# Performance work log

Hardware: AMD Instinct MI355X
Metric: run time of the kernel (lower is better)

Reference implementation:

```python
import jax, jax.numpy as jnp
import numpy as np

NUM_HEADS = 16
KERNEL_SIZE = 13


def setup_inputs() -> dict:
    key = jax.random.key(0)
    ks = jax.random.split(key, 6)
    B, L, C = 4, 4096, 512
    H, K = NUM_HEADS, KERNEL_SIZE
    x = jax.random.normal(ks[0], (B, L, C), dtype=jnp.float32)
    qkv_w = jax.random.normal(ks[1], (C, 3 * C), dtype=jnp.float32) * 0.02
    qkv_b = jnp.zeros((3 * C,), dtype=jnp.float32)
    rpb = jax.random.normal(ks[2], (H, 2 * K - 1), dtype=jnp.float32) * 0.02
    proj_w = jax.random.normal(ks[3], (C, C), dtype=jnp.float32) * 0.02
    proj_b = jnp.zeros((C,), dtype=jnp.float32)
    return {"x": x, "qkv_w": qkv_w, "qkv_b": qkv_b, "rpb": rpb,
            "proj_w": proj_w, "proj_b": proj_b}


def reference(x, qkv_w, qkv_b, rpb, proj_w, proj_b):
    B, L, C = x.shape
    H, K = NUM_HEADS, KERNEL_SIZE
    hd = C // H
    scale = hd ** -0.5
    kh = K // 2

    # qkv projection -> q,k,v each [B,H,L,hd]
    qkv = (x @ qkv_w + qkv_b).reshape(B, L, 3, H, hd).transpose(2, 0, 3, 1, 4)
    q, k, v = qkv[0] * scale, qkv[1], qkv[2]

    # NATTEN window: start index clamped so window stays in-bounds
    pos = jnp.arange(L)
    ni = jnp.clip(pos - kh, 0, L - K)              # [L] window start per query
    idx = ni[:, None] + jnp.arange(K)[None, :]     # [L,K] key positions
    # rpb index: (key_pos - query_pos) + (K-1)
    rpb_idx = (ni - pos + (K - 1))[:, None] + jnp.arange(K)[None, :]  # [L,K]

    k_win = k[:, :, idx, :]                        # [B,H,L,K,hd]
    v_win = v[:, :, idx, :]                        # [B,H,L,K,hd]

    attn = jnp.einsum('bhld,bhlkd->bhlk', q, k_win) + rpb[:, rpb_idx][None]
    attn = jax.nn.softmax(attn, axis=-1)

    out = jnp.einsum('bhlk,bhlkd->bhld', attn, v_win)  # [B,H,L,hd]
    out = out.transpose(0, 2, 1, 3).reshape(B, L, C)
    return out @ proj_w + proj_b
```

## Files before the change

### kernel.cpp

```cpp
#include <hip/hip_runtime.h>
#include <hip/hip_bf16.h>
#include <stdint.h>


typedef __attribute__((ext_vector_type(8))) short short8;
typedef __attribute__((ext_vector_type(4))) float f32x4;
typedef __attribute__((ext_vector_type(8))) unsigned short u16x8;
typedef __attribute__((ext_vector_type(4))) float float4v;

#define NB 4
#define NL 4096
#define NC 512
#define NH 16
#define HD 32
#define KW 13
#define KHALF 6
#define NM (NB*NL)

__device__ __forceinline__ float b2f(unsigned short u) {
  union { unsigned int i; float f; } x; x.i = ((unsigned int)u) << 16; return x.f;
}
__device__ __forceinline__ unsigned short f2b(float f) {
  __hip_bfloat16 h = __float2bfloat16(f);
  return __builtin_bit_cast(unsigned short, h);
}
__device__ __forceinline__ void gll16(const void* g, unsigned short* l) {
  __builtin_amdgcn_global_load_lds(
      (const __attribute__((address_space(1))) void*)g,
      (__attribute__((address_space(3))) void*)l, 16, 0, 0);
}
__device__ __forceinline__ short8 pack8(float4v lo, float4v hi) {
  u16x8 u;
  u[0] = f2b(lo.x); u[1] = f2b(lo.y); u[2] = f2b(lo.z); u[3] = f2b(lo.w);
  u[4] = f2b(hi.x); u[5] = f2b(hi.y); u[6] = f2b(hi.z); u[7] = f2b(hi.w);
  return __builtin_bit_cast(short8, u);
}

__global__ __launch_bounds__(256)
void pack_bf(const float* __restrict__ W, unsigned short* __restrict__ Bf,
             int N, int ngroups) {
  int g = blockIdx.x * 256 + threadIdx.x;
  if (g >= ngroups) return;
  int lane = g & 63;
  int kb   = (g >> 6) & 1;
  int nj   = (g >> 7) & 3;
  int wn   = (g >> 9) & 1;
  int kt   = (g >> 10) & 7;
  int tn   = g >> 13;
  int n  = tn * 128 + wn * 64 + nj * 16 + (lane & 15);
  int k0 = kt * 64 + (kb * 4 + (lane >> 4)) * 8;
  u16x8 u;
  #pragma unroll
  for (int e = 0; e < 8; ++e) u[e] = f2b(W[(long)(k0 + e) * N + n]);
  ((u16x8*)Bf)[g] = u;
}

#define BAR() __builtin_amdgcn_s_barrier()
#define LGK0() do { asm volatile("s_waitcnt lgkmcnt(0)" ::: "memory"); \
                    __builtin_amdgcn_sched_barrier(0); } while (0)
#define VM(N) asm volatile("s_waitcnt vmcnt(" #N ")" ::: "memory")

#define LDBG(KT) do { \
  const short8* _bp = (const short8*)(Bfw + (long)(KT) * 8192) + lane; \
  _Pragma("unroll") for (int nj = 0; nj < 4; ++nj) \
    _Pragma("unroll") for (int kb = 0; kb < 2; ++kb) \
      bf[nj][kb] = _bp[(nj*2 + kb) * 64]; \
} while (0)

#define MMA_ALL() do { \
  __builtin_amdgcn_s_setprio(1); \
  _Pragma("unroll") for (int ii = 0; ii < 4; ++ii) \
    _Pragma("unroll") for (int jj = 0; jj < 4; ++jj) \
      _Pragma("unroll") for (int kb = 0; kb < 2; ++kb) \
        acc[ii][jj] = __builtin_amdgcn_mfma_f32_16x16x32_bf16( \
            af[ii][kb], bf[jj][kb], acc[ii][jj], 0, 0, 0); \
  __builtin_amdgcn_s_setprio(0); \
} while (0)


__device__ __forceinline__ void stageA_f32(const float* __restrict__ G,
                                           long rowBase, int K, int kt,
                                           unsigned short* ldsDst, int tid) {
  int lane = tid & 63, w = tid >> 6;
  int rsub = lane >> 4;
  int slot = lane & 15;
  #pragma unroll
  for (int q = 0; q < 8; ++q) {
    int row = w * 32 + q * 4 + rsub;
    int g = slot ^ (row & 15);
    const float* src = G + (rowBase + row) * (long)K + kt * 64 + g * 4;
    gll16(src, ldsDst + row * 128 + slot * 8);
  }
}

#define LDA_F32(ABASE) do { \
  const char* _ba = (const char*)(ABASE); \
  _Pragma("unroll") for (int ii = 0; ii < 4; ++ii) { \
    int _row = wm*64 + ii*16 + lr; \
    const char* _rp = _ba + _row*256; \
    _Pragma("unroll") for (int kb = 0; kb < 2; ++kb) { \
      int _g = (kb*4 + lk) * 2; \
      float4v _lo = *(const float4v*)(_rp + ((_g ^ lr) * 16)); \
      float4v _hi = *(const float4v*)(_rp + (((_g+1) ^ lr) * 16)); \
      af[ii][kb] = pack8(_lo, _hi); \
    } \
  } \
} while (0)

#define G1TILE(ABUF, KT, STG, VMARG) do { \
  LDBG(KT); \
  LDA_F32(ABUF); \
  LGK0(); \
  BAR(); \
  if (STG) stageA_f32(Ag, mBase, K, (KT) + 2, ABUF, tid); \
  VMARG; \
  MMA_ALL(); \
  BAR(); \
} while (0)

__global__ __launch_bounds__(256, 2)
void gemm128f(const float* __restrict__ Ag,
              const unsigned short* __restrict__ Bf,
              const float* __restrict__ bias,
              unsigned short* __restrict__ Cout,
              int M, int N, int K, int tilesN) {
  __shared__ __align__(16) unsigned short lds[32768];

  int tid = threadIdx.x;
  int nwg = gridDim.x;
  int cpx = nwg >> 3;
  int wg  = ((int)blockIdx.x & 7) * cpx + ((int)blockIdx.x >> 3);
  int tm = wg / tilesN, tn = wg % tilesN;
  long mBase = (long)tm * 128;
  long nBase = (long)tn * 128;

  int lane = tid & 63, wave = tid >> 6;
  int wm = wave >> 1, wn = wave & 1;
  int lr = lane & 15, lk = lane >> 4;

  const unsigned short* Bfw = Bf + (long)tn * 65536 + wn * 4096;

  unsigned short* A0 = lds;
  unsigned short* A1 = lds + 16384;

  f32x4 acc[4][4];
  #pragma unroll
  for (int i = 0; i < 4; ++i)
    #pragma unroll
    for (int j = 0; j < 4; ++j) acc[i][j] = (f32x4){0.f, 0.f, 0.f, 0.f};

  short8 af[4][2], bf[4][2];

  stageA_f32(Ag, mBase, K, 0, A0, tid);
  stageA_f32(Ag, mBase, K, 1, A1, tid);
  VM(8);
  BAR();

  #pragma unroll 1
  for (int i = 0; i < 3; ++i) {
    G1TILE(A0, 2*i,     true, VM(8));
    G1TILE(A1, 2*i + 1, true, VM(8));
  }
  G1TILE(A0, 6, false, VM(0));
  G1TILE(A1, 7, false, VM(0));

  long rowb = mBase + wm * 64 + (lane >> 4) * 4;
  int  colb = (int)nBase + wn * 64 + lr;
  #pragma unroll
  for (int mi = 0; mi < 4; ++mi)
    #pragma unroll
    for (int nj = 0; nj < 4; ++nj) {
      int col = colb + nj * 16;
      float bv = bias[col];
      #pragma unroll
      for (int r = 0; r < 4; ++r)
        Cout[(rowb + mi * 16 + r) * (long)N + col] = f2b(acc[mi][nj][r] + bv);
    }
}

__device__ __forceinline__ void stage_tileA(const unsigned short* __restrict__ G,
                                            long rowBase, int K, int kt,
                                            unsigned short* ldsDst, int tid) {
  int r  = tid >> 3;
  int ch = (tid & 7) ^ (r & 7);
  const unsigned short* s0 = G + (rowBase + r) * (long)K + kt * 64 + ch * 8;
  unsigned short* d0 = ldsDst + tid * 8;
  #pragma unroll
  for (int q = 0; q < 4; ++q)
    gll16(s0 + (long)32 * q * K, d0 + 2048 * q);
}

#define LDA_B16(ABASE) do { \
  const char* _ba = (const char*)(ABASE); \
  _Pragma("unroll") for (int ii = 0; ii < 4; ++ii) { \
    int _row = wm*64 + ii*16 + lr; \
    _Pragma("unroll") for (int kb = 0; kb < 2; ++kb) \
      af[ii][kb] = *(const short8*)(_ba + _row*128 + (((kb*4+lk) ^ lr7) * 16)); \
  } \
} while (0)

#define G2TILE(ABUF, KT, STG, VMARG) do { \
  LDBG(KT); \
  LDA_B16(ABUF); \
  LGK0(); \
  BAR(); \
  if (STG) stage_tileA(Ag, mBase, K, (KT) + 2, ABUF, tid); \
  VMARG; \
  MMA_ALL(); \
  BAR(); \
} while (0)

__global__ __launch_bounds__(256, 3)
void gemm128b(const unsigned short* __restrict__ Ag,
              const unsigned short* __restrict__ Bf,
              const float* __restrict__ bias,
              float* __restrict__ Cout,
              int M, int N, int K, int tilesN) {
  __shared__ __align__(16) unsigned short lds[16384];

  int tid = threadIdx.x;
  int nwg = gridDim.x;
  int cpx = nwg >> 3;
  int wg  = ((int)blockIdx.x & 7) * cpx + ((int)blockIdx.x >> 3);
  int tm = wg / tilesN, tn = wg % tilesN;
  long mBase = (long)tm * 128;
  long nBase = (long)tn * 128;

  int lane = tid & 63, wave = tid >> 6;
  int wm = wave >> 1, wn = wave & 1;
  int lr = lane & 15, lk = lane >> 4, lr7 = lr & 7;

  const unsigned short* Bfw = Bf + (long)tn * 65536 + wn * 4096;

  unsigned short* A0 = lds;
  unsigned short* A1 = lds + 8192;

  f32x4 acc[4][4];
  #pragma unroll
  for (int i = 0; i < 4; ++i)
    #pragma unroll
    for (int j = 0; j < 4; ++j) acc[i][j] = (f32x4){0.f, 0.f, 0.f, 0.f};

  short8 af[4][2], bf[4][2];

  stage_tileA(Ag, mBase, K, 0, A0, tid);
  stage_tileA(Ag, mBase, K, 1, A1, tid);
  VM(4);
  BAR();

  #pragma unroll 1
  for (int i = 0; i < 3; ++i) {
    G2TILE(A0, 2*i,     true, VM(4));
    G2TILE(A1, 2*i + 1, true, VM(4));
  }
  G2TILE(A0, 6, false, VM(0));
  G2TILE(A1, 7, false, VM(0));

  long rowb = mBase + wm * 64 + (lane >> 4) * 4;
  int  colb = (int)nBase + wn * 64 + lr;
  #pragma unroll
  for (int mi = 0; mi < 4; ++mi)
    #pragma unroll
    for (int nj = 0; nj < 4; ++nj) {
      int col = colb + nj * 16;
      float bv = bias[col];
      #pragma unroll
      for (int r = 0; r < 4; ++r)
        Cout[(rowb + mi * 16 + r) * (long)N + col] = acc[mi][nj][r] + bv;
    }
}

__global__ __launch_bounds__(256)
void natt(const unsigned short* __restrict__ qkv, const float* __restrict__ rpb,
          unsigned short* __restrict__ out) {
  int tid = blockIdx.x * 256 + threadIdx.x;
  int h = tid & 15;
  int l = (tid >> 4) & (NL - 1);
  int b = tid >> 16;
  const float scale = 0.17677669529663687f;

  long qb = ((long)(b * NL + l) * 3) * NC + h * HD;
  float q[HD];
  {
    const u16x8* q8 = (const u16x8*)(qkv + qb);
    #pragma unroll
    for (int w = 0; w < 4; ++w) {
      u16x8 u = q8[w];
      #pragma unroll
      for (int e = 0; e < 8; ++e) q[w * 8 + e] = b2f(u[e]) * scale;
    }
  }

  int ni = l - KHALF;
  if (ni < 0) ni = 0;
  if (ni > NL - KW) ni = NL - KW;
  const float* rb = rpb + h * (2 * KW - 1) + (ni - l + KW - 1);

  float p[KW];
  float mx = -1e30f;
  #pragma unroll
  for (int j = 0; j < KW; ++j) {
    long kb = ((long)(b * NL + ni + j) * 3 + 1) * NC + h * HD;
    const u16x8* k8 = (const u16x8*)(qkv + kb);
    float s = 0.f;
    #pragma unroll
    for (int w = 0; w < 4; ++w) {
      u16x8 u = k8[w];
      #pragma unroll
      for (int e = 0; e < 8; ++e) s += q[w * 8 + e] * b2f(u[e]);
    }
    s += rb[j];
    p[j] = s;
    mx = fmaxf(mx, s);
  }

  float sum = 0.f;
  #pragma unroll
  for (int j = 0; j < KW; ++j) { p[j] = __expf(p[j] - mx); sum += p[j]; }
  float inv = 1.0f / sum;

  float o[HD];
  #pragma unroll
  for (int d = 0; d < HD; ++d) o[d] = 0.f;
  #pragma unroll
  for (int j = 0; j < KW; ++j) {
    long vb = ((long)(b * NL + ni + j) * 3 + 2) * NC + h * HD;
    const u16x8* v8 = (const u16x8*)(qkv + vb);
    float wj = p[j] * inv;
    #pragma unroll
    for (int w = 0; w < 4; ++w) {
      u16x8 u = v8[w];
      #pragma unroll
      for (int e = 0; e < 8; ++e) o[w * 8 + e] += wj * b2f(u[e]);
    }
  }

  unsigned short* op = out + (long)(b * NL + l) * NC + h * HD;
  #pragma unroll
  for (int w = 0; w < 4; ++w) {
    u16x8 u;
    #pragma unroll
    for (int e = 0; e < 8; ++e) u[e] = f2b(o[w * 8 + e]);
    *((u16x8*)(op + w * 8)) = u;
  }
}

extern "C" void kernel_launch(void* const* d_in, const int* in_sizes, int n_in,
                              void* d_out, int out_size, void* d_ws, size_t ws_size,
                              hipStream_t stream) {
  const float* x      = (const float*)d_in[0];
  const float* qkv_w  = (const float*)d_in[1];
  const float* qkv_b  = (const float*)d_in[2];
  const float* rpb    = (const float*)d_in[3];
  const float* proj_w = (const float*)d_in[4];
  const float* proj_b = (const float*)d_in[5];
  float* out = (float*)d_out;

  char* ws = (char*)d_ws;
  unsigned short* Bf1  = (unsigned short*)(ws);
  unsigned short* Bf2  = (unsigned short*)(ws + 1572864);
  unsigned short* qkvo = (unsigned short*)(ws + 2097152);
  unsigned short* attno= (unsigned short*)(ws + 52428800);

  pack_bf<<<dim3(384), dim3(256), 0, stream>>>(qkv_w, Bf1, 1536, 98304);
  pack_bf<<<dim3(128), dim3(256), 0, stream>>>(proj_w, Bf2, 512, 32768);
  gemm128f<<<dim3(1536), dim3(256), 0, stream>>>(x, Bf1, qkv_b, qkvo,
                                                 NM, 1536, 512, 12);
  natt<<<dim3(1024), dim3(256), 0, stream>>>(qkvo, rpb, attno);
  gemm128b<<<dim3(512), dim3(256), 0, stream>>>(attno, Bf2, proj_b, out,
                                                NM, 512, 512, 4);
}
```

Baseline: 103.4 us.

## Convert fp32 A tiles to bf16 once via registers before LDS staging

```diff
diff --git a/kernel.cpp b/kernel.cpp
--- a/kernel.cpp
+++ b/kernel.cpp
@@ -28,12 +28,6 @@
   __builtin_amdgcn_global_load_lds(
       (const __attribute__((address_space(1))) void*)g,
       (__attribute__((address_space(3))) void*)l, 16, 0, 0);
-}
-__device__ __forceinline__ short8 pack8(float4v lo, float4v hi) {
-  u16x8 u;
-  u[0] = f2b(lo.x); u[1] = f2b(lo.y); u[2] = f2b(lo.z); u[3] = f2b(lo.w);
-  u[4] = f2b(hi.x); u[5] = f2b(hi.y); u[6] = f2b(hi.z); u[7] = f2b(hi.w);
-  return __builtin_bit_cast(short8, u);
 }
 
 __global__ __launch_bounds__(256)
@@ -58,6 +52,7 @@
 #define BAR() __builtin_amdgcn_s_barrier()
 #define LGK0() do { asm volatile("s_waitcnt lgkmcnt(0)" ::: "memory"); \
                     __builtin_amdgcn_sched_barrier(0); } while (0)
+#define LGKW() asm volatile("s_waitcnt lgkmcnt(0)" ::: "memory")
 #define VM(N) asm volatile("s_waitcnt vmcnt(" #N ")" ::: "memory")
 
 #define LDBG(KT) do { \
@@ -65,6 +60,15 @@
   _Pragma("unroll") for (int nj = 0; nj < 4; ++nj) \
     _Pragma("unroll") for (int kb = 0; kb < 2; ++kb) \
       bf[nj][kb] = _bp[(nj*2 + kb) * 64]; \
+} while (0)
+
+#define LDA_B16(ABASE) do { \
+  const char* _ba = (const char*)(ABASE); \
+  _Pragma("unroll") for (int ii = 0; ii < 4; ++ii) { \
+    int _row = wm*64 + ii*16 + lr; \
+    _Pragma("unroll") for (int kb = 0; kb < 2; ++kb) \
+      af[ii][kb] = *(const short8*)(_ba + _row*128 + (((kb*4+lk) ^ lr7) * 16)); \
+  } \
 } while (0)
 
 #define MMA_ALL() do { \
@@ -78,44 +82,42 @@
 } while (0)
 
 
-__device__ __forceinline__ void stageA_f32(const float* __restrict__ G,
-                                           long rowBase, int K, int kt,
-                                           unsigned short* ldsDst, int tid) {
-  int lane = tid & 63, w = tid >> 6;
-  int rsub = lane >> 4;
-  int slot = lane & 15;
-  #pragma unroll
-  for (int q = 0; q < 8; ++q) {
-    int row = w * 32 + q * 4 + rsub;
-    int g = slot ^ (row & 15);
-    const float* src = G + (rowBase + row) * (long)K + kt * 64 + g * 4;
-    gll16(src, ldsDst + row * 128 + slot * 8);
-  }
-}
-
-#define LDA_F32(ABASE) do { \
-  const char* _ba = (const char*)(ABASE); \
-  _Pragma("unroll") for (int ii = 0; ii < 4; ++ii) { \
-    int _row = wm*64 + ii*16 + lr; \
-    const char* _rp = _ba + _row*256; \
-    _Pragma("unroll") for (int kb = 0; kb < 2; ++kb) { \
-      int _g = (kb*4 + lk) * 2; \
-      float4v _lo = *(const float4v*)(_rp + ((_g ^ lr) * 16)); \
-      float4v _hi = *(const float4v*)(_rp + (((_g+1) ^ lr) * 16)); \
-      af[ii][kb] = pack8(_lo, _hi); \
-    } \
-  } \
-} while (0)
-
-#define G1TILE(ABUF, KT, STG, VMARG) do { \
+__device__ __forceinline__ void loadA_f32(const float* __restrict__ G,
+                                          long rowBase, int K, int kt,
+                                          int tid, float4v (&ra)[8]) {
+  int r  = tid >> 3;
+  int ch = tid & 7;
+  const float* s = G + (rowBase + r) * (long)K + kt * 64 + ch * 8;
+  #pragma unroll
+  for (int q = 0; q < 4; ++q) {
+    const float4v* p = (const float4v*)(s + (long)32 * q * K);
+    ra[2 * q]     = p[0];
+    ra[2 * q + 1] = p[1];
+  }
+}
+__device__ __forceinline__ void writeA_bf16(unsigned short* ldsA, int tid,
+                                            const float4v (&ra)[8]) {
+  int r  = tid >> 3;
+  int ch = tid & 7;
+  #pragma unroll
+  for (int q = 0; q < 4; ++q) {
+    int row = r + 32 * q;
+    const float4v a = ra[2 * q], b = ra[2 * q + 1];
+    u16x8 u;
+    u[0] = f2b(a.x); u[1] = f2b(a.y); u[2] = f2b(a.z); u[3] = f2b(a.w);
+    u[4] = f2b(b.x); u[5] = f2b(b.y); u[6] = f2b(b.z); u[7] = f2b(b.w);
+    *(u16x8*)(ldsA + row * 64 + ((ch ^ (row & 7)) * 8)) = u;
+  }
+}
+
+#define G1TILE(ABUF, KT, STG) do { \
+  if (STG) loadA_f32(Ag, mBase, K, (KT) + 2, tid, ra); \
   LDBG(KT); \
-  LDA_F32(ABUF); \
+  LDA_B16(ABUF); \
   LGK0(); \
-  BAR(); \
-  if (STG) stageA_f32(Ag, mBase, K, (KT) + 2, ABUF, tid); \
-  VMARG; \
   MMA_ALL(); \
   BAR(); \
+  if (STG) { writeA_bf16(ABUF, tid, ra); LGKW(); } \
 } while (0)
 
 __global__ __launch_bounds__(256, 2)
@@ -124,7 +126,7 @@
               const float* __restrict__ bias,
               unsigned short* __restrict__ Cout,
               int M, int N, int K, int tilesN) {
-  __shared__ __align__(16) unsigned short lds[32768];
+  __shared__ __align__(16) unsigned short lds[16384];
 
   int tid = threadIdx.x;
   int nwg = gridDim.x;
@@ -136,12 +138,12 @@
 
   int lane = tid & 63, wave = tid >> 6;
   int wm = wave >> 1, wn = wave & 1;
-  int lr = lane & 15, lk = lane >> 4;
+  int lr = lane & 15, lk = lane >> 4, lr7 = lr & 7;
 
   const unsigned short* Bfw = Bf + (long)tn * 65536 + wn * 4096;
 
   unsigned short* A0 = lds;
-  unsigned short* A1 = lds + 16384;
+  unsigned short* A1 = lds + 8192;
 
   f32x4 acc[4][4];
   #pragma unroll
@@ -150,19 +152,21 @@
     for (int j = 0; j < 4; ++j) acc[i][j] = (f32x4){0.f, 0.f, 0.f, 0.f};
 
   short8 af[4][2], bf[4][2];
-
-  stageA_f32(Ag, mBase, K, 0, A0, tid);
-  stageA_f32(Ag, mBase, K, 1, A1, tid);
-  VM(8);
-  BAR();
+  float4v ra[8];
+
+  loadA_f32(Ag, mBase, K, 0, tid, ra);
+  writeA_bf16(A0, tid, ra);
+  loadA_f32(Ag, mBase, K, 1, tid, ra);
+  writeA_bf16(A1, tid, ra);
+  LGKW(); BAR();
 
   #pragma unroll 1
   for (int i = 0; i < 3; ++i) {
-    G1TILE(A0, 2*i,     true, VM(8));
-    G1TILE(A1, 2*i + 1, true, VM(8));
-  }
-  G1TILE(A0, 6, false, VM(0));
-  G1TILE(A1, 7, false, VM(0));
+    G1TILE(A0, 2*i,     true);
+    G1TILE(A1, 2*i + 1, true);
+  }
+  G1TILE(A0, 6, false);
+  G1TILE(A1, 7, false);
 
   long rowb = mBase + wm * 64 + (lane >> 4) * 4;
   int  colb = (int)nBase + wn * 64 + lr;
@@ -189,15 +193,6 @@
   for (int q = 0; q < 4; ++q)
     gll16(s0 + (long)32 * q * K, d0 + 2048 * q);
 }
-
-#define LDA_B16(ABASE) do { \
-  const char* _ba = (const char*)(ABASE); \
-  _Pragma("unroll") for (int ii = 0; ii < 4; ++ii) { \
-    int _row = wm*64 + ii*16 + lr; \
-    _Pragma("unroll") for (int kb = 0; kb < 2; ++kb) \
-      af[ii][kb] = *(const short8*)(_ba + _row*128 + (((kb*4+lk) ^ lr7) * 16)); \
-  } \
-} while (0)
 
 #define G2TILE(ABUF, KT, STG, VMARG) do { \
   LDBG(KT); \
```

Result: faster. 101.1 us (-2.2%).
